# Kernel optimization log

Hardware: AMD Instinct MI355X
Metric: run time of the kernel (lower is better)

The kernel has to match this reference:

```python
import jax, jax.numpy as jnp
import numpy as np

B, M, IN_DIM = 8, 2048, 512
N_HEAD, ATTN_DIM = 8, 64
HEAD_DIM = N_HEAD * ATTN_DIM  # 512
SCALE = HEAD_DIM ** (-0.5)


def setup_inputs() -> dict:
    key = jax.random.key(0)
    ks = jax.random.split(key, 5)
    s = IN_DIM ** -0.5
    return {
        "x": jax.random.normal(ks[0], (B, M, IN_DIM), dtype=jnp.float32),
        "Wq": jax.random.normal(ks[1], (IN_DIM, HEAD_DIM), dtype=jnp.float32) * s,
        "Wk": jax.random.normal(ks[2], (IN_DIM, HEAD_DIM), dtype=jnp.float32) * s,
        "Wv": jax.random.normal(ks[3], (IN_DIM, HEAD_DIM), dtype=jnp.float32) * s,
        "Wo": jax.random.normal(ks[4], (HEAD_DIM, IN_DIM), dtype=jnp.float32) * s,
        "bo": jnp.zeros((IN_DIM,), dtype=jnp.float32),
    }


def _split_heads(t):
    # [B, M, H*D] -> [B, H, M, D]
    b, m, _ = t.shape
    return t.reshape(b, m, N_HEAD, ATTN_DIM).transpose(0, 2, 1, 3)


def reference(x, Wq, Wk, Wv, Wo, bo):
    q = _split_heads(x @ Wq)  # bhmd
    k = _split_heads(x @ Wk)
    v = _split_heads(x @ Wv)
    # Faithful to source: logits DIVIDED by scale=head_dim**-0.5 (i.e. * sqrt(head_dim))
    logits = jnp.einsum('bhid,bhjd->bhij', q, k) / SCALE
    scores = jax.nn.softmax(logits, axis=-1)
    weighted = jnp.einsum('bhij,bhjd->bhid', scores, v)  # [B,H,M,D]
    merged = weighted.transpose(0, 2, 1, 3).reshape(x.shape[0], x.shape[1], HEAD_DIM)
    return merged @ Wo + bo
```

## Files before the change

kernel.cpp:

```cpp
#include <hip/hip_runtime.h>
#include <hip/hip_bf16.h>
#include <cstdint>

#define DI __device__ __forceinline__

typedef __attribute__((ext_vector_type(8))) short bf16x8;
typedef __attribute__((ext_vector_type(4))) short s16x4;
typedef __attribute__((ext_vector_type(4))) float f32x4;

static constexpr int BATCH = 8, SEQ = 2048;
static constexpr int ROWS = BATCH * SEQ;
static constexpr float SCALE_Q = (float)(22.627416997969522 * 1.4426950408889634);

DI short f2bf(float f) { __hip_bfloat16 h = __float2bfloat16(f); return *reinterpret_cast<short*>(&h); }
DI float bf2f(short s) { __hip_bfloat16 h; *reinterpret_cast<short*>(&h) = s; return __bfloat162float(h); }

DI void gload_lds16(const void* gp, void* lp) {
  __builtin_amdgcn_global_load_lds(
      (__attribute__((address_space(1))) void*)const_cast<void*>(gp),
      (__attribute__((address_space(3))) void*)lp, 16, 0, 0);
}
DI f32x4 mfma16(bf16x8 a, bf16x8 b, f32x4 c) {
  return __builtin_amdgcn_mfma_f32_16x16x32_bf16(a, b, c, 0, 0, 0);
}

__global__ __launch_bounds__(256)
void prep_w(const float* __restrict__ Wq, const float* __restrict__ Wk,
            const float* __restrict__ Wv, const float* __restrict__ Wo,
            short* __restrict__ Wqk_hi, short* __restrict__ Wqk_lo,
            short* __restrict__ Wv_t, short* __restrict__ Wo_t)
{
  __shared__ float t[64][65];
  const int blk = blockIdx.x;
  const int mat = blk >> 6;
  const int tile = blk & 63;
  const int tn = (tile & 7) * 64;
  const int tk = (tile >> 3) * 64;
  const float* src = mat == 0 ? Wq : mat == 1 ? Wk : mat == 2 ? Wv : Wo;
  const float scale = (mat == 0) ? SCALE_Q : 1.0f;
  const int tid = threadIdx.x;
#pragma unroll
  for (int i = 0; i < 16; ++i) {
    int idx = i * 256 + tid;
    t[idx >> 6][idx & 63] = src[(size_t)(tk + (idx >> 6)) * 512 + tn + (idx & 63)];
  }
  __syncthreads();
#pragma unroll
  for (int i = 0; i < 16; ++i) {
    int idx = i * 256 + tid;
    int nn = idx >> 6, kk = idx & 63;
    float v = t[kk][nn] * scale;
    short hb = f2bf(v);
    size_t o = (size_t)(tn + nn) * 512 + (tk + kk);
    if (mat <= 1) {
      Wqk_hi[(size_t)mat * 512 * 512 + o] = hb;
      Wqk_lo[(size_t)mat * 512 * 512 + o] = f2bf(v - bf2f(hb));
    } else if (mat == 2) Wv_t[o] = hb;
    else Wo_t[o] = hb;
  }
}

template<int MODE>
__global__ __launch_bounds__(256, 2)
void gemm_kern(const float* __restrict__ Axf, const short* __restrict__ Axb,
               const short* __restrict__ Bhg, const short* __restrict__ Blg,
               short* __restrict__ O0h, short* __restrict__ O0l,
               short* __restrict__ O1h, short* __restrict__ O1l,
               float* __restrict__ Of, const float* __restrict__ bias)
{
  constexpr bool SPLIT = (MODE == 0);
  __shared__ __align__(16) short Ah[128 * 32];
  __shared__ __align__(16) short Bh[128 * 32];
  __shared__ __align__(16) short Al[SPLIT ? 128 * 32 : 16];
  __shared__ __align__(16) short Bl[SPLIT ? 128 * 32 : 16];

  const int tid = threadIdx.x;
  const int wave = tid >> 6, lane = tid & 63, lo = lane & 15, hi4 = lane >> 4;
  const int wr = wave >> 1, wc = wave & 1;
  const int m0 = blockIdx.y * 128, n0 = blockIdx.x * 128;

  f32x4 acc[4][4] = {};

  for (int kt = 0; kt < 16; ++kt) {
    __syncthreads();
    if constexpr (MODE != 2) {
#pragma unroll
      for (int r2 = 0; r2 < 4; ++r2) {
        int idx = r2 * 256 + tid;
        int row = idx >> 3, c4 = idx & 7;
        const float4 v = *reinterpret_cast<const float4*>(Axf + (size_t)(m0 + row) * 512 + kt * 32 + c4 * 4);
        s16x4 h4, l4;
#pragma unroll
        for (int j = 0; j < 4; ++j) {
          float f = ((const float*)&v)[j];
          short hb = f2bf(f);
          h4[j] = hb;
          if constexpr (SPLIT) l4[j] = f2bf(f - bf2f(hb));
        }
        int off = row * 64 + ((((c4 >> 1) ^ ((row >> 1) & 3)) << 4) | ((c4 & 1) << 3));
        *reinterpret_cast<s16x4*>((char*)Ah + off) = h4;
        if constexpr (SPLIT) *reinterpret_cast<s16x4*>((char*)Al + off) = l4;
      }
    } else {
#pragma unroll
      for (int is = 0; is < 2; ++is) {
        int rowl = is * 64 + wave * 16 + (lane >> 2);
        int chunk = (lane & 3) ^ ((rowl >> 1) & 3);
        const char* src = (const char*)Axb + ((size_t)(m0 + rowl) * 512 + kt * 32) * 2 + chunk * 16;
        gload_lds16(src, (char*)Ah + is * 4096 + wave * 1024);
      }
    }
#pragma unroll
    for (int is = 0; is < 2; ++is) {
      int rowl = is * 64 + wave * 16 + (lane >> 2);
      int chunk = (lane & 3) ^ ((rowl >> 1) & 3);
      size_t gb = ((size_t)(n0 + rowl) * 512 + kt * 32) * 2 + chunk * 16;
      gload_lds16((const char*)Bhg + gb, (char*)Bh + is * 4096 + wave * 1024);
      if constexpr (SPLIT)
        gload_lds16((const char*)Blg + gb, (char*)Bl + is * 4096 + wave * 1024);
    }
    __syncthreads();
    bf16x8 a_h[4], a_l[4], b_h[4], b_l[4];
#pragma unroll
    for (int m = 0; m < 4; ++m) {
      int ar = wr * 64 + m * 16 + lo;
      int off = ar * 64 + ((hi4 ^ ((ar >> 1) & 3)) << 4);
      a_h[m] = *reinterpret_cast<const bf16x8*>((const char*)Ah + off);
      if constexpr (SPLIT) a_l[m] = *reinterpret_cast<const bf16x8*>((const char*)Al + off);
    }
#pragma unroll
    for (int n = 0; n < 4; ++n) {
      int br = wc * 64 + n * 16 + lo;
      int off = br * 64 + ((hi4 ^ ((br >> 1) & 3)) << 4);
      b_h[n] = *reinterpret_cast<const bf16x8*>((const char*)Bh + off);
      if constexpr (SPLIT) b_l[n] = *reinterpret_cast<const bf16x8*>((const char*)Bl + off);
    }
#pragma unroll
    for (int m = 0; m < 4; ++m)
#pragma unroll
      for (int n = 0; n < 4; ++n) {
        acc[m][n] = mfma16(a_h[m], b_h[n], acc[m][n]);
        if constexpr (SPLIT) {
          acc[m][n] = mfma16(a_h[m], b_l[n], acc[m][n]);
          acc[m][n] = mfma16(a_l[m], b_h[n], acc[m][n]);
        }
      }
  }
#pragma unroll
  for (int m = 0; m < 4; ++m)
#pragma unroll
    for (int n = 0; n < 4; ++n) {
      if constexpr (MODE == 1) {
        int cg = n0 + wc * 64 + n * 16 + lo;
        int rgb = m0 + wr * 64 + m * 16 + hi4 * 4;
        int bh = (rgb >> 11) * 8 + (cg >> 6);
        s16x4 vt4;
#pragma unroll
        for (int j = 0; j < 4; ++j) vt4[j] = f2bf(acc[m][n][j]);
        size_t o = ((size_t)(bh * 64 + (cg & 63))) * 2048 + (rgb & 2047);
        *reinterpret_cast<s16x4*>(O0h + o) = vt4;
      } else {
#pragma unroll
        for (int j = 0; j < 4; ++j) {
          int rg = m0 + wr * 64 + m * 16 + hi4 * 4 + j;
          int cg = n0 + wc * 64 + n * 16 + lo;
          float v = acc[m][n][j];
          if constexpr (MODE == 2) {
            Of[(size_t)rg * 512 + cg] = v + bias[cg];
          } else {
            int mat = cg >> 9;
            int c9 = cg & 511;
            size_t o = ((size_t)((rg >> 11) * 8 + (c9 >> 6)) * 2048 + (rg & 2047)) * 64 + (c9 & 63);
            short hb = f2bf(v);
            short lb = f2bf(v - bf2f(hb));
            if (mat == 0) { O0h[o] = hb; O0l[o] = lb; }
            else          { O1h[o] = hb; O1l[o] = lb; }
          }
        }
      }
    }
}

__global__ __launch_bounds__(256, 2)
void attn_kern(const short* __restrict__ Qh, const short* __restrict__ Ql,
               const short* __restrict__ Kh, const short* __restrict__ Kl,
               const short* __restrict__ VTg, short* __restrict__ Og)
{
  __shared__ __align__(16) short Ksh[64 * 64];
  __shared__ __align__(16) short Ksl[64 * 64];
  __shared__ __align__(16) short Vts[64 * 64];
  __shared__ __align__(16) short Ps[4][1024];

  const int bh = blockIdx.y, qt = blockIdx.x;
  const int tid = threadIdx.x, wave = tid >> 6, lane = tid & 63, lo = lane & 15, hi4 = lane >> 4;
  const int q0 = qt * 64;

  const size_t qoff = ((size_t)bh * 2048 + q0 + wave * 16 + lo) * 64;
  bf16x8 qh[2], ql[2];
#pragma unroll
  for (int kk = 0; kk < 2; ++kk) {
    qh[kk] = *reinterpret_cast<const bf16x8*>(Qh + qoff + kk * 32 + hi4 * 8);
    ql[kk] = *reinterpret_cast<const bf16x8*>(Ql + qoff + kk * 32 + hi4 * 8);
  }

  f32x4 acc_o[4] = {};
  float m_run[4], l_run[4];
#pragma unroll
  for (int j = 0; j < 4; ++j) { m_run[j] = -3.0e38f; l_run[j] = 0.f; }

  short* pw = &Ps[wave][0];

  for (int kt = 0; kt < 32; ++kt) {
    __syncthreads();
#pragma unroll
    for (int is = 0; is < 2; ++is) {
      int rowl = is * 32 + wave * 8 + (lane >> 3);
      int chunk = (lane & 7) ^ (rowl & 7);
      size_t gbK = ((size_t)bh * 2048 + kt * 64 + rowl) * 128 + chunk * 16;
      gload_lds16((const char*)Kh + gbK, (char*)Ksh + is * 4096 + wave * 1024);
      gload_lds16((const char*)Kl + gbK, (char*)Ksl + is * 4096 + wave * 1024);
      size_t gbV = (((size_t)bh * 64 + rowl) * 2048 + kt * 64) * 2 + chunk * 16;
      gload_lds16((const char*)VTg + gbV, (char*)Vts + is * 4096 + wave * 1024);
    }
    __syncthreads();

    f32x4 s[4];
#pragma unroll
    for (int kb = 0; kb < 4; ++kb) {
      f32x4 t = {0.f, 0.f, 0.f, 0.f};
#pragma unroll
      for (int kk = 0; kk < 2; ++kk) {
        int krow = kb * 16 + lo;
        int off = krow * 128 + ((kk * 64 + hi4 * 16) ^ ((krow & 7) << 4));
        bf16x8 kh8 = *reinterpret_cast<const bf16x8*>((const char*)Ksh + off);
        bf16x8 kl8 = *reinterpret_cast<const bf16x8*>((const char*)Ksl + off);
        t = mfma16(qh[kk], kh8, t);
        t = mfma16(qh[kk], kl8, t);
        t = mfma16(ql[kk], kh8, t);
      }
      s[kb] = t;
    }

    float mt[4];
#pragma unroll
    for (int j = 0; j < 4; ++j)
      mt[j] = fmaxf(fmaxf(s[0][j], s[1][j]), fmaxf(s[2][j], s[3][j]));
#pragma unroll
    for (int d = 1; d <= 8; d <<= 1) {
#pragma unroll
      for (int j = 0; j < 4; ++j) mt[j] = fmaxf(mt[j], __shfl_xor(mt[j], d));
    }
    float corr[4], ls[4];
#pragma unroll
    for (int j = 0; j < 4; ++j) {
      float mn = fmaxf(m_run[j], mt[j]);
      corr[j] = exp2f(m_run[j] - mn);
      m_run[j] = mn;
      ls[j] = 0.f;
    }
#pragma unroll
    for (int kb = 0; kb < 4; ++kb)
#pragma unroll
      for (int j = 0; j < 4; ++j) {
        float p = exp2f(s[kb][j] - m_run[j]);
        s[kb][j] = p;
        ls[j] += p;
      }
#pragma unroll
    for (int d = 1; d <= 8; d <<= 1) {
#pragma unroll
      for (int j = 0; j < 4; ++j) ls[j] += __shfl_xor(ls[j], d);
    }
#pragma unroll
    for (int j = 0; j < 4; ++j) l_run[j] = l_run[j] * corr[j] + ls[j];
#pragma unroll
    for (int db = 0; db < 4; ++db)
#pragma unroll
      for (int j = 0; j < 4; ++j) acc_o[db][j] *= corr[j];

#pragma unroll
    for (int kb = 0; kb < 4; ++kb)
#pragma unroll
      for (int j = 0; j < 4; ++j) {
        int row = hi4 * 4 + j, col = kb * 16 + lo;
        int off = row * 128 + ((col * 2) ^ ((row & 7) << 4));
        *reinterpret_cast<short*>((char*)pw + off) = f2bf(s[kb][j]);
      }
    __builtin_amdgcn_sched_barrier(0);
    bf16x8 pa[2];
#pragma unroll
    for (int kk = 0; kk < 2; ++kk) {
      int off = lo * 128 + ((kk * 64 + hi4 * 16) ^ ((lo & 7) << 4));
      pa[kk] = *reinterpret_cast<const bf16x8*>((const char*)pw + off);
    }

#pragma unroll
    for (int db = 0; db < 4; ++db) {
#pragma unroll
      for (int kk = 0; kk < 2; ++kk) {
        int vrow = db * 16 + lo;
        int voff = vrow * 128 + ((kk * 64 + hi4 * 16) ^ ((lo & 7) << 4));
        bf16x8 v8 = *reinterpret_cast<const bf16x8*>((const char*)Vts + voff);
        acc_o[db] = mfma16(pa[kk], v8, acc_o[db]);
      }
    }
  }

  const int b = bh >> 3, h = bh & 7;
#pragma unroll
  for (int j = 0; j < 4; ++j) {
    float inv = 1.0f / l_run[j];
    int mrow = q0 + wave * 16 + hi4 * 4 + j;
    size_t base = ((size_t)(b * 2048 + mrow)) * 512 + h * 64;
#pragma unroll
    for (int db = 0; db < 4; ++db)
      Og[base + db * 16 + lo] = f2bf(acc_o[db][j] * inv);
  }
}

extern "C" void kernel_launch(void* const* d_in, const int* in_sizes, int n_in,
                              void* d_out, int out_size, void* d_ws, size_t ws_size,
                              hipStream_t stream) {
  const float* x  = (const float*)d_in[0];
  const float* Wq = (const float*)d_in[1];
  const float* Wk = (const float*)d_in[2];
  const float* Wv = (const float*)d_in[3];
  const float* Wo = (const float*)d_in[4];
  const float* bo = (const float*)d_in[5];
  float* out = (float*)d_out;

  char* ws = (char*)d_ws;
  short* Wqk_hi = (short*)(ws);
  short* Wqk_lo = (short*)(ws + (1 << 20));
  short* Wv_t   = (short*)(ws + (2 << 20));
  short* Wo_t   = (short*)(ws + (2 << 20) + 512 * 512 * 2);
  char* big = ws + 3 * (1 << 20);
  const size_t SZ = (size_t)ROWS * 512 * 2;
  short* Qh = (short*)(big);
  short* Ql = (short*)(big + SZ);
  short* Kh = (short*)(big + 2 * SZ);
  short* Kl = (short*)(big + 3 * SZ);
  short* VT = (short*)(big + 4 * SZ);
  short* Ob = (short*)(big + 5 * SZ);
  (void)in_sizes; (void)n_in; (void)out_size; (void)ws_size;

  prep_w<<<dim3(256), dim3(256), 0, stream>>>(Wq, Wk, Wv, Wo, Wqk_hi, Wqk_lo, Wv_t, Wo_t);
  gemm_kern<0><<<dim3(8, 128), dim3(256), 0, stream>>>(x, nullptr, Wqk_hi, Wqk_lo,
                                                       Qh, Ql, Kh, Kl, nullptr, nullptr);
  gemm_kern<1><<<dim3(4, 128), dim3(256), 0, stream>>>(x, nullptr, Wv_t, nullptr,
                                                       VT, nullptr, nullptr, nullptr, nullptr, nullptr);
  attn_kern<<<dim3(32, 64), dim3(256), 0, stream>>>(Qh, Ql, Kh, Kl, VT, Ob);
  gemm_kern<2><<<dim3(4, 128), dim3(256), 0, stream>>>(nullptr, Ob, Wo_t, nullptr,
                                                       nullptr, nullptr, nullptr, nullptr, out, bo);
}
```

Measured before the change: 463.9 us.

## Transpose QK^T MFMA layout, add lazy softmax rescaling and packed P stores

```diff
diff --git a/kernel.cpp b/kernel.cpp
--- a/kernel.cpp
+++ b/kernel.cpp
@@ -7,6 +7,7 @@
 typedef __attribute__((ext_vector_type(8))) short bf16x8;
 typedef __attribute__((ext_vector_type(4))) short s16x4;
 typedef __attribute__((ext_vector_type(4))) float f32x4;
+typedef __attribute__((ext_vector_type(2))) int   i32x2;
 
 static constexpr int BATCH = 8, SEQ = 2048;
 static constexpr int ROWS = BATCH * SEQ;
@@ -14,6 +15,9 @@
 
 DI short f2bf(float f) { __hip_bfloat16 h = __float2bfloat16(f); return *reinterpret_cast<short*>(&h); }
 DI float bf2f(short s) { __hip_bfloat16 h; *reinterpret_cast<short*>(&h) = s; return __bfloat162float(h); }
+DI unsigned pack2(float a, float b) {
+  return (unsigned)(unsigned short)f2bf(a) | ((unsigned)(unsigned short)f2bf(b) << 16);
+}
 
 DI void gload_lds16(const void* gp, void* lp) {
   __builtin_amdgcn_global_load_lds(
@@ -204,9 +208,7 @@
   }
 
   f32x4 acc_o[4] = {};
-  float m_run[4], l_run[4];
-#pragma unroll
-  for (int j = 0; j < 4; ++j) { m_run[j] = -3.0e38f; l_run[j] = 0.f; }
+  float m_run = -3.0e38f, l_run = 0.f;
 
   short* pw = &Ps[wave][0];
 
@@ -225,6 +227,7 @@
     __syncthreads();
 
     f32x4 s[4];
+    __builtin_amdgcn_s_setprio(1);
 #pragma unroll
     for (int kb = 0; kb < 4; ++kb) {
       f32x4 t = {0.f, 0.f, 0.f, 0.f};
@@ -234,58 +237,54 @@
         int off = krow * 128 + ((kk * 64 + hi4 * 16) ^ ((krow & 7) << 4));
         bf16x8 kh8 = *reinterpret_cast<const bf16x8*>((const char*)Ksh + off);
         bf16x8 kl8 = *reinterpret_cast<const bf16x8*>((const char*)Ksl + off);
-        t = mfma16(qh[kk], kh8, t);
-        t = mfma16(qh[kk], kl8, t);
-        t = mfma16(ql[kk], kh8, t);
+        t = mfma16(kh8, qh[kk], t);
+        t = mfma16(kl8, qh[kk], t);
+        t = mfma16(kh8, ql[kk], t);
       }
       s[kb] = t;
     }
-
-    float mt[4];
-#pragma unroll
-    for (int j = 0; j < 4; ++j)
-      mt[j] = fmaxf(fmaxf(s[0][j], s[1][j]), fmaxf(s[2][j], s[3][j]));
-#pragma unroll
-    for (int d = 1; d <= 8; d <<= 1) {
-#pragma unroll
-      for (int j = 0; j < 4; ++j) mt[j] = fmaxf(mt[j], __shfl_xor(mt[j], d));
-    }
-    float corr[4], ls[4];
-#pragma unroll
-    for (int j = 0; j < 4; ++j) {
-      float mn = fmaxf(m_run[j], mt[j]);
-      corr[j] = exp2f(m_run[j] - mn);
-      m_run[j] = mn;
-      ls[j] = 0.f;
-    }
+    __builtin_amdgcn_s_setprio(0);
+
+    float mt = s[0][0];
 #pragma unroll
     for (int kb = 0; kb < 4; ++kb)
 #pragma unroll
+      for (int j = 0; j < 4; ++j) mt = fmaxf(mt, s[kb][j]);
+    mt = fmaxf(mt, __shfl_xor(mt, 16));
+    mt = fmaxf(mt, __shfl_xor(mt, 32));
+    if (!__all(mt - m_run <= 8.0f)) {
+      float mn = fmaxf(m_run, mt);
+      float corr = exp2f(m_run - mn);
+      m_run = mn;
+      l_run *= corr;
+#pragma unroll
       for (int j = 0; j < 4; ++j) {
-        float p = exp2f(s[kb][j] - m_run[j]);
+        float cj = __shfl(corr, hi4 * 4 + j);
+#pragma unroll
+        for (int db = 0; db < 4; ++db) acc_o[db][j] *= cj;
+      }
+    }
+    float ls = 0.f;
+#pragma unroll
+    for (int kb = 0; kb < 4; ++kb)
+#pragma unroll
+      for (int j = 0; j < 4; ++j) {
+        float p = exp2f(s[kb][j] - m_run);
         s[kb][j] = p;
-        ls[j] += p;
-      }
-#pragma unroll
-    for (int d = 1; d <= 8; d <<= 1) {
-#pragma unroll
-      for (int j = 0; j < 4; ++j) ls[j] += __shfl_xor(ls[j], d);
-    }
-#pragma unroll
-    for (int j = 0; j < 4; ++j) l_run[j] = l_run[j] * corr[j] + ls[j];
-#pragma unroll
-    for (int db = 0; db < 4; ++db)
-#pragma unroll
-      for (int j = 0; j < 4; ++j) acc_o[db][j] *= corr[j];
-
-#pragma unroll
-    for (int kb = 0; kb < 4; ++kb)
-#pragma unroll
-      for (int j = 0; j < 4; ++j) {
-        int row = hi4 * 4 + j, col = kb * 16 + lo;
-        int off = row * 128 + ((col * 2) ^ ((row & 7) << 4));
-        *reinterpret_cast<short*>((char*)pw + off) = f2bf(s[kb][j]);
-      }
+        ls += p;
+      }
+    ls += __shfl_xor(ls, 16);
+    ls += __shfl_xor(ls, 32);
+    l_run += ls;
+
+#pragma unroll
+    for (int kb = 0; kb < 4; ++kb) {
+      i32x2 w;
+      w.x = (int)pack2(s[kb][0], s[kb][1]);
+      w.y = (int)pack2(s[kb][2], s[kb][3]);
+      int off = lo * 128 + ((kb * 32 + hi4 * 8) ^ ((lo & 7) << 4));
+      *reinterpret_cast<i32x2*>((char*)pw + off) = w;
+    }
     __builtin_amdgcn_sched_barrier(0);
     bf16x8 pa[2];
 #pragma unroll
@@ -294,6 +293,7 @@
       pa[kk] = *reinterpret_cast<const bf16x8*>((const char*)pw + off);
     }
 
+    __builtin_amdgcn_s_setprio(1);
 #pragma unroll
     for (int db = 0; db < 4; ++db) {
 #pragma unroll
@@ -304,12 +304,14 @@
         acc_o[db] = mfma16(pa[kk], v8, acc_o[db]);
       }
     }
+    __builtin_amdgcn_s_setprio(0);
   }
 
   const int b = bh >> 3, h = bh & 7;
 #pragma unroll
   for (int j = 0; j < 4; ++j) {
-    float inv = 1.0f / l_run[j];
+    float lr = __shfl(l_run, hi4 * 4 + j);
+    float inv = 1.0f / lr;
     int mrow = q0 + wave * 16 + hi4 * 4 + j;
     size_t base = ((size_t)(b * 2048 + mrow)) * 512 + h * 64;
 #pragma unroll
```

Result: faster. 402.2 us (-13.3%).
